# Optimization experiments

Hardware: AMD Instinct MI355X
Metric: run time of the kernel (lower is better)

The kernel has to match this reference:

```python
import jax, jax.numpy as jnp
import numpy as np

HIDDEN = 2880
NUM_EXPERTS = 32
TOP_K = 4


def setup_inputs() -> dict:
    key = jax.random.key(0)
    k1, k2, k3 = jax.random.split(key, 3)
    hidden_states = jax.random.normal(k1, (4, 4096, HIDDEN), dtype=jnp.float32)
    weight = jax.random.normal(k2, (NUM_EXPERTS, HIDDEN), dtype=jnp.float32) * (1.0 / np.sqrt(HIDDEN))
    bias = jax.random.normal(k3, (NUM_EXPERTS,), dtype=jnp.float32) * 0.02
    return {"hidden_states": hidden_states, "weight": weight, "bias": bias}


def reference(hidden_states, weight, bias):
    # flatten tokens: [T, H]
    x = hidden_states.reshape(-1, HIDDEN)
    # router logits: [T, E]
    router_logits = jnp.einsum('th,eh->te', x, weight) + bias
    # top-k selection along experts
    top_vals, top_idx = jax.lax.top_k(router_logits, TOP_K)  # [T, K]
    top_vals = jax.nn.softmax(top_vals, axis=-1)
    # scatter normalized scores back into a zero [T, E] tensor
    T = router_logits.shape[0]
    rows = jnp.arange(T)[:, None]
    router_scores = jnp.zeros_like(router_logits).at[rows, top_idx].set(top_vals)
    return router_scores, top_idx
```

## Files before the change

kernel.cpp:

```cpp
#include <hip/hip_runtime.h>
#include <math.h>


#define HIDDEN 2880
#define NE 32
#define TOPK 4
#define TPB 32
#define NK16 192
#define RK16 180
#define VS (NK16 * 512)

typedef __attribute__((ext_vector_type(8)))  short bf16x8;
typedef __attribute__((ext_vector_type(16))) float f32x16;

#define MFMA32(a, b, c) __builtin_amdgcn_mfma_f32_32x32x16_bf16((a), (b), (c), 0, 0, 0)

__global__ void wb_kernel(const float* __restrict__ w, unsigned short* __restrict__ wb) {
    int i = blockIdx.x * 256 + threadIdx.x;
    if (i >= 3 * VS) return;
    int j = i & 7;
    int l = (i >> 3) & 63;
    int rest = i >> 9;
    int ks  = rest % NK16;
    int ver = rest / NK16;
    unsigned short outv = 0;
    if (ks < RK16) {
        int e = l & 31;
        int k = ks * 16 + (l >> 5) * 8 + j;
        float v = w[e * HIDDEN + k];
        unsigned u = __float_as_uint(v);
        unsigned h = u >> 16;
        float r = v - __uint_as_float(u & 0xffff0000u);
        unsigned ur = __float_as_uint(r);
        unsigned m = ur >> 16;
        float r2 = r - __uint_as_float(ur & 0xffff0000u);
        unsigned lo = __float_as_uint(r2) >> 16;
        outv = (unsigned short)(ver == 0 ? h : (ver == 1 ? m : lo));
    }
    wb[i] = outv;
}

__device__ __forceinline__ void split24(float4 a, float4 b,
                                        bf16x8& H, bf16x8& M, bf16x8& L) {
    union { bf16x8 v; unsigned u[4]; } h, m, l;
    float f[8] = {a.x, a.y, a.z, a.w, b.x, b.y, b.z, b.w};
    unsigned hh[8], mm[8], ll[8];
#pragma unroll
    for (int i = 0; i < 8; ++i) {
        unsigned u = __float_as_uint(f[i]);
        hh[i] = u >> 16;
        float r = f[i] - __uint_as_float(u & 0xffff0000u);
        unsigned ur = __float_as_uint(r);
        mm[i] = ur >> 16;
        float r2 = r - __uint_as_float(ur & 0xffff0000u);
        ll[i] = __float_as_uint(r2) >> 16;
    }
#pragma unroll
    for (int i = 0; i < 4; ++i) {
        h.u[i] = hh[2 * i] | (hh[2 * i + 1] << 16);
        m.u[i] = mm[2 * i] | (mm[2 * i + 1] << 16);
        l.u[i] = ll[2 * i] | (ll[2 * i + 1] << 16);
    }
    H = h.v; M = m.v; L = l.v;
}

__global__ __launch_bounds__(512, 4)
void router_kernel(const float* __restrict__ x,
                   const unsigned short* __restrict__ wb,
                   const float* __restrict__ bias,
                   float* __restrict__ out_scores,
                   float* __restrict__ out_idx)
{
    __shared__ float part[8][TPB][36];
    __shared__ float score[TPB][33];

    const int tid  = threadIdx.x;
    const int lane = tid & 63;
    const int w    = tid >> 6;
    const int col  = lane & 31;
    const int kg   = lane >> 5;

    const float* xrow = x + (size_t)(blockIdx.x * TPB + col) * HIDDEN + kg * 8;
    const unsigned short* wk = wb + lane * 8;

    f32x16 acc = {0.f};

#define LOADX(A0, A1, sg) do {                                                    \
    const int sx_ = min((sg), RK16 - 1);                                          \
    A0 = *(const float4*)(xrow + (size_t)sx_ * 16);                               \
    A1 = *(const float4*)(xrow + (size_t)sx_ * 16 + 4);                           \
} while (0)

#define LOADW(W3, sg) do {                                                        \
    const unsigned short* p_ = wk + (size_t)min((sg), NK16 - 1) * 512;            \
    W3[0] = *(const bf16x8*)(p_);                                        \
    W3[1] = *(const bf16x8*)(p_ + VS);                                   \
    W3[2] = *(const bf16x8*)(p_ + 2 * VS);                               \
} while (0)

#define MFMA6(W3, XH, XM, XL) do {                                                \
    acc = MFMA32(W3[0], XH, acc);                                                 \
    acc = MFMA32(W3[1], XH, acc);                                                 \
    acc = MFMA32(W3[2], XH, acc);                                                 \
    acc = MFMA32(W3[0], XM, acc);                                                 \
    acc = MFMA32(W3[1], XM, acc);                                                 \
    acc = MFMA32(W3[0], XL, acc);                                                 \
} while (0)

#define PHASE(XB0, XB1, WB3, s, P) do {                                           \
    bf16x8 xh_, xm_, xl_;                                                         \
    split24(XB0, XB1, xh_, xm_, xl_);                                             \
    LOADX(XB0, XB1, (s) + (P) + 4);                                               \
    MFMA6(WB3, xh_, xm_, xl_);                                                    \
    LOADW(WB3, (s) + (P) + 2);                                                    \
} while (0)

    const int sg0 = w * 24;
    float4 x0a, x0b, x1a, x1b, x2a, x2b, x3a, x3b;
    bf16x8 Wa[3], Wb[3];
    LOADX(x0a, x0b, sg0);
    LOADX(x1a, x1b, sg0 + 1);
    LOADX(x2a, x2b, sg0 + 2);
    LOADX(x3a, x3b, sg0 + 3);
    LOADW(Wa, sg0);
    LOADW(Wb, sg0 + 1);

#pragma unroll 1
    for (int i = 0; i < 6; ++i) {
        const int s = sg0 + 4 * i;
        PHASE(x0a, x0b, Wa, s, 0);
        PHASE(x1a, x1b, Wb, s, 1);
        PHASE(x2a, x2b, Wa, s, 2);
        PHASE(x3a, x3b, Wb, s, 3);
    }

#undef LOADX
#undef LOADW
#undef MFMA6
#undef PHASE

#pragma unroll
    for (int r = 0; r < 16; ++r)
        part[w][col][(r & 3) + 8 * (r >> 2) + 4 * kg] = acc[r];
    __syncthreads();

    if (tid < TPB) {
        float lg[NE];
#pragma unroll
        for (int e = 0; e < NE; ++e) {
            float s = bias[e];
#pragma unroll
            for (int p = 0; p < 8; ++p) s += part[p][tid][e];
            lg[e] = s;
        }

        float vals[TOPK]; int idxs[TOPK]; unsigned chosen = 0u;
#pragma unroll
        for (int k = 0; k < TOPK; ++k) {
            float m = -INFINITY; int mi = 0;
#pragma unroll
            for (int e = 0; e < NE; ++e) {
                const bool take = (((chosen >> e) & 1u) == 0u) && (lg[e] > m);
                m  = take ? lg[e] : m;
                mi = take ? e : mi;
            }
            vals[k] = m; idxs[k] = mi; chosen |= (1u << (unsigned)mi);
        }
        const float mx = vals[0];
        float p[TOPK]; float sum = 0.f;
#pragma unroll
        for (int k = 0; k < TOPK; ++k) { p[k] = __expf(vals[k] - mx); sum += p[k]; }
        const float inv = 1.0f / sum;
#pragma unroll
        for (int e = 0; e < NE; ++e) {
            float v = 0.f;
#pragma unroll
            for (int k = 0; k < TOPK; ++k) v = (e == idxs[k]) ? p[k] * inv : v;
            score[tid][e] = v;
        }
        const int t = blockIdx.x * TPB + tid;
        float4 iv = make_float4((float)idxs[0], (float)idxs[1], (float)idxs[2], (float)idxs[3]);
        *reinterpret_cast<float4*>(out_idx + (size_t)t * TOPK) = iv;
    }
    __syncthreads();

    {
        const int f = tid * 2;
        const int t = f >> 5, e = f & 31;
        float2 v = make_float2(score[t][e], score[t][e + 1]);
        *reinterpret_cast<float2*>(out_scores + (size_t)blockIdx.x * TPB * NE + f) = v;
    }
}

extern "C" void kernel_launch(void* const* d_in, const int* in_sizes, int n_in,
                              void* d_out, int out_size, void* d_ws, size_t ws_size,
                              hipStream_t stream)
{
    const float* x = (const float*)d_in[0];
    const float* w = (const float*)d_in[1];
    const float* b = (const float*)d_in[2];
    const int T = in_sizes[0] / HIDDEN;

    unsigned short* wbuf = (unsigned short*)d_ws;
    float* out        = (float*)d_out;
    float* out_scores = out;
    float* out_idx    = out + (size_t)T * NE;

    wb_kernel<<<dim3((3 * VS + 255) / 256), dim3(256), 0, stream>>>(w, wbuf);
    router_kernel<<<dim3(T / TPB), dim3(512), 0, stream>>>(x, wbuf, b, out_scores, out_idx);
}
```

Baseline: 55.88 us.

## Stage x through double-buffered swizzled LDS chunks with coalesced global loads

```diff
diff --git a/kernel.cpp b/kernel.cpp
--- a/kernel.cpp
+++ b/kernel.cpp
@@ -6,8 +6,10 @@
 #define NE 32
 #define TOPK 4
 #define TPB 32
-#define NK16 192
-#define RK16 180
+#define CKF 192
+#define SPC 12
+#define NCH 15
+#define NK16 180
 #define VS (NK16 * 512)
 
 typedef __attribute__((ext_vector_type(8)))  short bf16x8;
@@ -23,21 +25,17 @@
     int rest = i >> 9;
     int ks  = rest % NK16;
     int ver = rest / NK16;
-    unsigned short outv = 0;
-    if (ks < RK16) {
-        int e = l & 31;
-        int k = ks * 16 + (l >> 5) * 8 + j;
-        float v = w[e * HIDDEN + k];
-        unsigned u = __float_as_uint(v);
-        unsigned h = u >> 16;
-        float r = v - __uint_as_float(u & 0xffff0000u);
-        unsigned ur = __float_as_uint(r);
-        unsigned m = ur >> 16;
-        float r2 = r - __uint_as_float(ur & 0xffff0000u);
-        unsigned lo = __float_as_uint(r2) >> 16;
-        outv = (unsigned short)(ver == 0 ? h : (ver == 1 ? m : lo));
-    }
-    wb[i] = outv;
+    int e = l & 31;
+    int k = ks * 16 + (l >> 5) * 8 + j;
+    float v = w[e * HIDDEN + k];
+    unsigned u = __float_as_uint(v);
+    unsigned h = u >> 16;
+    float r = v - __uint_as_float(u & 0xffff0000u);
+    unsigned ur = __float_as_uint(r);
+    unsigned m = ur >> 16;
+    float r2 = r - __uint_as_float(ur & 0xffff0000u);
+    unsigned lo = __float_as_uint(r2) >> 16;
+    wb[i] = (unsigned short)(ver == 0 ? h : (ver == 1 ? m : lo));
 }
 
 __device__ __forceinline__ void split24(float4 a, float4 b,
@@ -71,73 +69,120 @@
                    float* __restrict__ out_scores,
                    float* __restrict__ out_idx)
 {
-    __shared__ float part[8][TPB][36];
-    __shared__ float score[TPB][33];
+    __shared__ float pool[2 * TPB * CKF];
+    float* buf0 = pool;
+    float* buf1 = pool + TPB * CKF;
 
     const int tid  = threadIdx.x;
     const int lane = tid & 63;
     const int w    = tid >> 6;
     const int col  = lane & 31;
     const int kg   = lane >> 5;
-
-    const float* xrow = x + (size_t)(blockIdx.x * TPB + col) * HIDDEN + kg * 8;
+    const int tok0 = blockIdx.x * TPB;
+
+    const float* xg[3];
+    int wi[3];
+#pragma unroll
+    for (int i = 0; i < 3; ++i) {
+        int f    = i * 512 + tid;
+        int grow = f / 48;
+        int gcol = f - grow * 48;
+        xg[i] = x + (size_t)(tok0 + grow) * HIDDEN + gcol * 4;
+        wi[i] = grow * CKF + ((gcol ^ (grow & 15)) << 2);
+    }
+
+    const int rbase = col * CKF;
+    const int rx    = col & 15;
     const unsigned short* wk = wb + lane * 8;
 
     f32x16 acc = {0.f};
-
-#define LOADX(A0, A1, sg) do {                                                    \
-    const int sx_ = min((sg), RK16 - 1);                                          \
-    A0 = *(const float4*)(xrow + (size_t)sx_ * 16);                               \
-    A1 = *(const float4*)(xrow + (size_t)sx_ * 16 + 4);                           \
-} while (0)
-
-#define LOADW(W3, sg) do {                                                        \
-    const unsigned short* p_ = wk + (size_t)min((sg), NK16 - 1) * 512;            \
-    W3[0] = *(const bf16x8*)(p_);                                        \
-    W3[1] = *(const bf16x8*)(p_ + VS);                                   \
-    W3[2] = *(const bf16x8*)(p_ + 2 * VS);                               \
-} while (0)
-
-#define MFMA6(W3, XH, XM, XL) do {                                                \
-    acc = MFMA32(W3[0], XH, acc);                                                 \
-    acc = MFMA32(W3[1], XH, acc);                                                 \
-    acc = MFMA32(W3[2], XH, acc);                                                 \
-    acc = MFMA32(W3[0], XM, acc);                                                 \
-    acc = MFMA32(W3[1], XM, acc);                                                 \
-    acc = MFMA32(W3[0], XL, acc);                                                 \
-} while (0)
-
-#define PHASE(XB0, XB1, WB3, s, P) do {                                           \
-    bf16x8 xh_, xm_, xl_;                                                         \
-    split24(XB0, XB1, xh_, xm_, xl_);                                             \
-    LOADX(XB0, XB1, (s) + (P) + 4);                                               \
-    MFMA6(WB3, xh_, xm_, xl_);                                                    \
-    LOADW(WB3, (s) + (P) + 2);                                                    \
-} while (0)
-
-    const int sg0 = w * 24;
-    float4 x0a, x0b, x1a, x1b, x2a, x2b, x3a, x3b;
-    bf16x8 Wa[3], Wb[3];
-    LOADX(x0a, x0b, sg0);
-    LOADX(x1a, x1b, sg0 + 1);
-    LOADX(x2a, x2b, sg0 + 2);
-    LOADX(x3a, x3b, sg0 + 3);
-    LOADW(Wa, sg0);
-    LOADW(Wb, sg0 + 1);
+    float4 gA[3], gB[3];
+
+#define GLOAD(g, c) do { _Pragma("unroll")                                        \
+    for (int i_ = 0; i_ < 3; ++i_)                                                \
+        g[i_] = *(const float4*)(xg[i_] + (size_t)(c) * CKF);                     \
+} while (0)
+
+#define SWRITE(dst, g) do { _Pragma("unroll")                                     \
+    for (int i_ = 0; i_ < 3; ++i_)                                                \
+        *(float4*)((dst) + wi[i_]) = g[i_];                                       \
+} while (0)
+
+#define BARW() do {                                                               \
+    asm volatile("s_waitcnt lgkmcnt(0)" ::: "memory");                            \
+    __builtin_amdgcn_s_barrier();                                                 \
+    asm volatile("" ::: "memory");                                                \
+} while (0)
+
+#define MFMA6(WH, WM, WL, XH, XM, XL) do {                                        \
+    acc = MFMA32(WH, XH, acc);                                                    \
+    acc = MFMA32(WM, XH, acc);                                                    \
+    acc = MFMA32(WL, XH, acc);                                                    \
+    acc = MFMA32(WH, XM, acc);                                                    \
+    acc = MFMA32(WM, XM, acc);                                                    \
+    acc = MFMA32(WH, XL, acc);                                                    \
+} while (0)
+
+#define COMPUTE(buf, c) do {                                                      \
+    const int sl0_ = (w + 4 * (c)) & 7;                                           \
+    const int g0_  = (c) * SPC + sl0_;                                            \
+    const bool two_ = sl0_ < 4;                                                   \
+    const unsigned short* p0_ = wk + (size_t)g0_ * 512;                           \
+    bf16x8 W0h = *(const bf16x8*)(p0_);                                           \
+    bf16x8 W0m = *(const bf16x8*)(p0_ + VS);                                      \
+    bf16x8 W0l = *(const bf16x8*)(p0_ + 2 * VS);                                  \
+    const int sA_ = sl0_ * 4 + kg * 2;                                            \
+    float4 a0_ = *(const float4*)((buf) + rbase + ((sA_)     ^ rx) * 4);          \
+    float4 a1_ = *(const float4*)((buf) + rbase + ((sA_ + 1) ^ rx) * 4);          \
+    if (two_) {                                                                   \
+        const unsigned short* p1_ = p0_ + 8 * 512;                                \
+        bf16x8 W1h = *(const bf16x8*)(p1_);                                       \
+        bf16x8 W1m = *(const bf16x8*)(p1_ + VS);                                  \
+        bf16x8 W1l = *(const bf16x8*)(p1_ + 2 * VS);                              \
+        const int sB_ = sA_ + 32;                                                 \
+        float4 b0_ = *(const float4*)((buf) + rbase + ((sB_)     ^ rx) * 4);      \
+        float4 b1_ = *(const float4*)((buf) + rbase + ((sB_ + 1) ^ rx) * 4);      \
+        bf16x8 xh_, xm_, xl_;                                                     \
+        split24(a0_, a1_, xh_, xm_, xl_);                                         \
+        MFMA6(W0h, W0m, W0l, xh_, xm_, xl_);                                      \
+        split24(b0_, b1_, xh_, xm_, xl_);                                         \
+        MFMA6(W1h, W1m, W1l, xh_, xm_, xl_);                                      \
+    } else {                                                                      \
+        bf16x8 xh_, xm_, xl_;                                                     \
+        split24(a0_, a1_, xh_, xm_, xl_);                                         \
+        MFMA6(W0h, W0m, W0l, xh_, xm_, xl_);                                      \
+    }                                                                             \
+} while (0)
+
+    GLOAD(gA, 0);
+    GLOAD(gB, 1);
+    SWRITE(buf0, gA);
+    GLOAD(gA, 2);
+    BARW();
 
 #pragma unroll 1
-    for (int i = 0; i < 6; ++i) {
-        const int s = sg0 + 4 * i;
-        PHASE(x0a, x0b, Wa, s, 0);
-        PHASE(x1a, x1b, Wb, s, 1);
-        PHASE(x2a, x2b, Wa, s, 2);
-        PHASE(x3a, x3b, Wb, s, 3);
-    }
-
-#undef LOADX
-#undef LOADW
+    for (int cc = 0; cc < 7; ++cc) {
+        const int c0 = 2 * cc;
+        COMPUTE(buf0, c0);
+        SWRITE(buf1, gB);
+        if (cc < 6) GLOAD(gB, c0 + 3);
+        BARW();
+        COMPUTE(buf1, c0 + 1);
+        SWRITE(buf0, gA);
+        if (cc < 6) GLOAD(gA, c0 + 4);
+        BARW();
+    }
+    COMPUTE(buf0, 14);
+    __syncthreads();
+
+#undef GLOAD
+#undef SWRITE
+#undef BARW
 #undef MFMA6
-#undef PHASE
+#undef COMPUTE
+
+    float (*part)[TPB][36] = (float (*)[TPB][36])pool;
+    float (*score)[33]     = (float (*)[33])(pool + 9216);
 
 #pragma unroll
     for (int r = 0; r < 16; ++r)
```

After: 88.84 us. 59.0% more time.

## Stage hidden-state chunks through per-wave LDS tiles with coalesced row loads

Applied to the files above, without the earlier changes.

```diff
diff --git a/kernel.cpp b/kernel.cpp
--- a/kernel.cpp
+++ b/kernel.cpp
@@ -9,6 +9,8 @@
 #define NK16 192
 #define RK16 180
 #define VS (NK16 * 512)
+#define ROWF 68
+#define NCHW 6
 
 typedef __attribute__((ext_vector_type(8)))  short bf16x8;
 typedef __attribute__((ext_vector_type(16))) float f32x16;
@@ -71,73 +73,85 @@
                    float* __restrict__ out_scores,
                    float* __restrict__ out_idx)
 {
-    __shared__ float part[8][TPB][36];
-    __shared__ float score[TPB][33];
+    __shared__ float pool[8 * TPB * ROWF];
 
     const int tid  = threadIdx.x;
     const int lane = tid & 63;
     const int w    = tid >> 6;
     const int col  = lane & 31;
     const int kg   = lane >> 5;
-
-    const float* xrow = x + (size_t)(blockIdx.x * TPB + col) * HIDDEN + kg * 8;
+    const int tok0 = blockIdx.x * TPB;
+
+    float* tile = pool + w * (TPB * ROWF);
+
+    const int srow  = lane >> 4;
+    const int sslot = lane & 15;
+    const float* xsrc = x + (size_t)(tok0 + srow) * HIDDEN;
+    float* sdst = tile + srow * ROWF + sslot * 4;
+
     const unsigned short* wk = wb + lane * 8;
 
     f32x16 acc = {0.f};
 
-#define LOADX(A0, A1, sg) do {                                                    \
-    const int sx_ = min((sg), RK16 - 1);                                          \
-    A0 = *(const float4*)(xrow + (size_t)sx_ * 16);                               \
-    A1 = *(const float4*)(xrow + (size_t)sx_ * 16 + 4);                           \
-} while (0)
-
-#define LOADW(W3, sg) do {                                                        \
-    const unsigned short* p_ = wk + (size_t)min((sg), NK16 - 1) * 512;            \
-    W3[0] = *(const bf16x8*)(p_);                                        \
-    W3[1] = *(const bf16x8*)(p_ + VS);                                   \
-    W3[2] = *(const bf16x8*)(p_ + 2 * VS);                               \
-} while (0)
-
-#define MFMA6(W3, XH, XM, XL) do {                                                \
-    acc = MFMA32(W3[0], XH, acc);                                                 \
-    acc = MFMA32(W3[1], XH, acc);                                                 \
-    acc = MFMA32(W3[2], XH, acc);                                                 \
-    acc = MFMA32(W3[0], XM, acc);                                                 \
-    acc = MFMA32(W3[1], XM, acc);                                                 \
-    acc = MFMA32(W3[0], XL, acc);                                                 \
-} while (0)
-
-#define PHASE(XB0, XB1, WB3, s, P) do {                                           \
+#define GLOAD(g, c) do { _Pragma("unroll")                                        \
+    for (int i_ = 0; i_ < 8; ++i_) {                                              \
+        int ko_ = min(384 * w + 64 * (c) + sslot * 4, HIDDEN - 4);                \
+        g[i_] = *(const float4*)(xsrc + (size_t)(4 * i_) * HIDDEN + ko_);         \
+    }                                                                             \
+} while (0)
+
+#define SWRITE(g) do { _Pragma("unroll")                                          \
+    for (int i_ = 0; i_ < 8; ++i_)                                                \
+        *(float4*)(sdst + 4 * i_ * ROWF) = g[i_];                                 \
+} while (0)
+
+#define MFMA6(WH, WM, WL, XH, XM, XL) do {                                        \
+    acc = MFMA32(WH, XH, acc);                                                    \
+    acc = MFMA32(WM, XH, acc);                                                    \
+    acc = MFMA32(WL, XH, acc);                                                    \
+    acc = MFMA32(WH, XM, acc);                                                    \
+    acc = MFMA32(WM, XM, acc);                                                    \
+    acc = MFMA32(WH, XL, acc);                                                    \
+} while (0)
+
+#define STEP(c, s) do {                                                           \
+    const int ro_ = col * ROWF + (s) * 16 + kg * 8;                               \
+    float4 a0_ = *(const float4*)(tile + ro_);                                    \
+    float4 a1_ = *(const float4*)(tile + ro_ + 4);                                \
+    const unsigned short* p_ = wk + (size_t)(24 * w + 4 * (c) + (s)) * 512;       \
+    bf16x8 Wh_ = *(const bf16x8*)(p_);                                            \
+    bf16x8 Wm_ = *(const bf16x8*)(p_ + VS);                                       \
+    bf16x8 Wl_ = *(const bf16x8*)(p_ + 2 * VS);                                   \
     bf16x8 xh_, xm_, xl_;                                                         \
-    split24(XB0, XB1, xh_, xm_, xl_);                                             \
-    LOADX(XB0, XB1, (s) + (P) + 4);                                               \
-    MFMA6(WB3, xh_, xm_, xl_);                                                    \
-    LOADW(WB3, (s) + (P) + 2);                                                    \
-} while (0)
-
-    const int sg0 = w * 24;
-    float4 x0a, x0b, x1a, x1b, x2a, x2b, x3a, x3b;
-    bf16x8 Wa[3], Wb[3];
-    LOADX(x0a, x0b, sg0);
-    LOADX(x1a, x1b, sg0 + 1);
-    LOADX(x2a, x2b, sg0 + 2);
-    LOADX(x3a, x3b, sg0 + 3);
-    LOADW(Wa, sg0);
-    LOADW(Wb, sg0 + 1);
+    split24(a0_, a1_, xh_, xm_, xl_);                                             \
+    MFMA6(Wh_, Wm_, Wl_, xh_, xm_, xl_);                                          \
+} while (0)
+
+    float4 g[8];
+
+    GLOAD(g, 0);
+    SWRITE(g);
+    GLOAD(g, 1);
 
 #pragma unroll 1
-    for (int i = 0; i < 6; ++i) {
-        const int s = sg0 + 4 * i;
-        PHASE(x0a, x0b, Wa, s, 0);
-        PHASE(x1a, x1b, Wb, s, 1);
-        PHASE(x2a, x2b, Wa, s, 2);
-        PHASE(x3a, x3b, Wb, s, 3);
-    }
-
-#undef LOADX
-#undef LOADW
+    for (int c = 0; c < NCHW; ++c) {
+#pragma unroll
+        for (int s = 0; s < 4; ++s) STEP(c, s);
+        if (c < NCHW - 1) {
+            SWRITE(g);
+            if (c < NCHW - 2) GLOAD(g, c + 2);
+        }
+    }
+
+#undef GLOAD
+#undef SWRITE
 #undef MFMA6
-#undef PHASE
+#undef STEP
+
+    __syncthreads();
+
+    float (*part)[TPB][36] = (float (*)[TPB][36])pool;
+    float (*score)[33]     = (float (*)[33])(pool + 8 * TPB * 36);
 
 #pragma unroll
     for (int r = 0; r < 16; ++r)
```

Measured after the change: 97.69 us. +74.8%, slower.
